# Optimization experiments

Measured on AMD Instinct MI355X. Metric: run time of the kernel, lower is better.

The kernel has to match this reference:

```python
import jax, jax.numpy as jnp
import numpy as np
from jax import lax


def conv1x1(x, w, b):
    # x: [B,C,H,W], w: [O,C], b: [O]
    return jnp.einsum('bchw,oc->bohw', x, w) + b[None, :, None, None]


def dwconv3(x, w, b):
    # depthwise 3x3, SAME padding. x: [B,C,H,W], w: [C,1,3,3], b: [C]
    C = x.shape[1]
    y = lax.conv_general_dilated(x, w, (1, 1), 'SAME',
                                 dimension_numbers=('NCHW', 'OIHW', 'NCHW'),
                                 feature_group_count=C)
    return y + b[None, :, None, None]


def proj(x, w1, b1, wd, bd):
    return dwconv3(conv1x1(x, w1, b1), wd, bd)


def setup_inputs() -> dict:
    key = jax.random.key(0)
    B, C, H, W = 8, 96, 256, 256
    ks = jax.random.split(key, 32)
    s = 0.05

    def rn(k, shape, scale=s):
        return jax.random.normal(k, shape, dtype=jnp.float32) * scale

    inp = {
        'I1': jax.random.normal(ks[0], (B, H * W, C), dtype=jnp.float32),
        'I2': jax.random.normal(ks[1], (B, H * W, C), dtype=jnp.float32),
        'h': H, 'w': W,
        'se1_w': rn(ks[2], (C, C)), 'se1_b': rn(ks[3], (C,)),
        'se1_dw': rn(ks[4], (C, 1, 3, 3)), 'se1_db': rn(ks[5], (C,)),
        'se2_w': rn(ks[6], (C, C)), 'se2_b': rn(ks[7], (C,)),
        'se2_dw': rn(ks[8], (C, 1, 3, 3)), 'se2_db': rn(ks[9], (C,)),
        'lp1_w': rn(ks[10], (C, C)), 'lp1_b': rn(ks[11], (C,)),
        'lp1_dw': rn(ks[12], (C, 1, 3, 3)), 'lp1_db': rn(ks[13], (C,)),
        'rp1_w': rn(ks[14], (C, C)), 'rp1_b': rn(ks[15], (C,)),
        'rp1_dw': rn(ks[16], (C, 1, 3, 3)), 'rp1_db': rn(ks[17], (C,)),
        'lp2_w': rn(ks[18], (C, C)), 'lp2_b': rn(ks[19], (C,)),
        'rp2_w': rn(ks[20], (C, C)), 'rp2_b': rn(ks[21], (C,)),
        'down_w': rn(ks[22], (C, 2 * C)), 'down_b': rn(ks[23], (C,)),
        'beta': rn(ks[24], (1, C, 1, 1), 0.1),
        'gamma': rn(ks[25], (1, C, 1, 1), 0.1),
    }
    return inp


def reference(I1, I2, h, w, se1_w, se1_b, se1_dw, se1_db, se2_w, se2_b,
              se2_dw, se2_db, lp1_w, lp1_b, lp1_dw, lp1_db, rp1_w, rp1_b,
              rp1_dw, rp1_db, lp2_w, lp2_b, rp2_w, rp2_b, down_w, down_b,
              beta, gamma):
    B, HW, C = I1.shape
    scale = C ** (-0.5)
    # PatchUnEmbed: [B, HW, C] -> [B, C, h, w]
    x_l = jnp.transpose(I1, (0, 2, 1)).reshape(B, C, h, w)
    x_r = jnp.transpose(I2, (0, 2, 1)).reshape(B, C, h, w)

    Q_l = jnp.transpose(proj(x_l, se1_w, se1_b, se1_dw, se1_db), (0, 2, 3, 1))  # [B,H,W,C]
    Q_r = jnp.transpose(proj(x_r, se2_w, se2_b, se2_dw, se2_db), (0, 2, 3, 1))  # [B,H,W,C]
    V_l = jnp.transpose(proj(x_l, lp1_w, lp1_b, lp1_dw, lp1_db), (0, 2, 3, 1))
    V_r = jnp.transpose(proj(x_r, rp1_w, rp1_b, rp1_dw, rp1_db), (0, 2, 3, 1))

    # row-wise cross attention along width: [B,H,W,W]
    attn = jax.nn.softmax(jnp.einsum('bhwc,bhvc->bhwv', Q_l, Q_r), axis=-1) * scale
    F_r2l = jnp.einsum('bhwv,bhvc->bhwc', attn, V_r)  # [B,H,W,C]
    F_l2r = jnp.einsum('bhwv,bhwc->bhvc', attn, V_l)  # attn^T @ V_l

    F_r2l = conv1x1(jnp.transpose(F_r2l, (0, 3, 1, 2)), lp2_w, lp2_b) * beta
    F_l2r = conv1x1(jnp.transpose(F_l2r, (0, 3, 1, 2)), rp2_w, rp2_b) * gamma

    fuse = conv1x1(jnp.concatenate([x_l + F_r2l, x_r + F_l2r], axis=1), down_w, down_b)
    # [B,C,H,W] -> [B, HW, C]
    return jnp.transpose(fuse.reshape(B, C, HW), (0, 2, 1))
```

## Files before the change

kernel.cpp:

```cpp
#include <hip/hip_runtime.h>
#include <hip/hip_bf16.h>
#include <stdint.h>

typedef __bf16 bf;
typedef __bf16 bfv8 __attribute__((ext_vector_type(8)));
typedef __bf16 bfv4 __attribute__((ext_vector_type(4)));
typedef float  f32x4 __attribute__((ext_vector_type(4)));

#define MFMA16(a,b,c) __builtin_amdgcn_mfma_f32_16x16x32_bf16((a),(b),(c),0,0,0)

#define CH  96
#define WID 256
#define HGT 256
#define NB  8
#define SCALE 0.1020620726159658f

__device__ __forceinline__ float b2f(bf x){ return (float)x; }
__device__ __forceinline__ bf   f2b(float x){ return (bf)x; }

__device__ __forceinline__ bfv8 ld_cvt8(const float* __restrict__ p){
  f32x4 a = *(const f32x4*)p;
  f32x4 b = *(const f32x4*)(p + 4);
  bfv8 r;
  r[0]=f2b(a[0]); r[1]=f2b(a[1]); r[2]=f2b(a[2]); r[3]=f2b(a[3]);
  r[4]=f2b(b[0]); r[5]=f2b(b[1]); r[6]=f2b(b[2]); r[7]=f2b(b[3]);
  return r;
}

__global__ __launch_bounds__(256) void k_c1x1(
    const float* __restrict__ X,
    const float* __restrict__ Wa, const float* __restrict__ Ba,
    const float* __restrict__ Wb, const float* __restrict__ Bb,
    bf* __restrict__ Ca, bf* __restrict__ Cb)
{
  const int tid=threadIdx.x, lane=tid&63, wv=tid>>6;
  const int l15=lane&15, lg=lane>>4;
  const int set = wv&1, th = wv>>1;
  const float* W1 = set ? Wb : Wa;
  const float* B1 = set ? Bb : Ba;
  bf* C = set ? Cb : Ca;
  const size_t p0 = (size_t)blockIdx.x * 256;

  bfv8 wf[6][3];
  float bias[6];
#pragma unroll
  for (int nt=0;nt<6;++nt){
    bias[nt] = B1[nt*16+l15];
#pragma unroll
    for (int ks=0;ks<3;++ks)
      wf[nt][ks] = ld_cvt8(W1 + (nt*16+l15)*CH + ks*32 + lg*8);
  }

#pragma unroll 1
  for (int i=0;i<8;++i){
    const int m0 = (th*8+i)*16;
    bfv8 af[3];
#pragma unroll
    for (int ks=0;ks<3;++ks)
      af[ks] = ld_cvt8(X + (p0+m0+l15)*CH + ks*32 + lg*8);
    f32x4 acc[6];
#pragma unroll
    for (int nt=0;nt<6;++nt) acc[nt]=(f32x4){bias[nt],bias[nt],bias[nt],bias[nt]};
#pragma unroll
    for (int ks=0;ks<3;++ks)
#pragma unroll
      for (int nt=0;nt<6;++nt)
        acc[nt] = MFMA16(af[ks], wf[nt][ks], acc[nt]);
#pragma unroll
    for (int nt=0;nt<6;++nt){
      int c = nt*16 + l15;
#pragma unroll
      for (int r=0;r<4;++r)
        C[(p0+m0+lg*4+r)*CH + c] = f2b(acc[nt][r]);
    }
  }
}

__global__ __launch_bounds__(256) void k_dw(
    const bf* __restrict__ C0, const bf* __restrict__ C1,
    const float* __restrict__ WD0, const float* __restrict__ BD0,
    const float* __restrict__ WD1, const float* __restrict__ BD1,
    bf* __restrict__ O0, bf* __restrict__ O1)
{
  const int tid = threadIdx.x;
  if (tid >= 240) return;
  const int g = tid % 12, slot = tid / 12;
  const int yrow = slot >> 2, xrun = slot & 3;
  const int b = blockIdx.z >> 1, s = blockIdx.z & 1;
  const bf* C = s ? C1 : C0;
  const float* WD = s ? WD1 : WD0;
  const float* BD = s ? BD1 : BD0;
  bf* O = s ? O1 : O0;
  const int x0 = blockIdx.x*64 + xrun*16;
  const int y  = blockIdx.y*5 + yrow;
  if (y >= HGT) return;
  const size_t ib = (size_t)b * (HGT*WID) * CH;

  float wv[9][8], bb[8];
#pragma unroll
  for (int j=0;j<8;++j){
    bb[j] = BD[g*8+j];
#pragma unroll
    for (int t=0;t<9;++t) wv[t][j] = WD[(g*8+j)*9 + t];
  }

  const bf* r0 = C + ib + ((size_t)(y-1)*WID)*CH + g*8;
  const bf* r1 = C + ib + ((size_t)(y  )*WID)*CH + g*8;
  const bf* r2 = C + ib + ((size_t)(y+1)*WID)*CH + g*8;
  const bool v0 = (y > 0), v2 = (y+1 < HGT);
  const bfv8 Z = {0,0,0,0,0,0,0,0};

  bfv8 w00,w01,w02, w10,w11,w12, w20,w21,w22;
  {
    bool vx = (x0 > 0);
    size_t o = (size_t)(x0-1)*CH;
    w00 = (v0&&vx) ? *(const bfv8*)(r0+o) : Z;
    w10 = vx       ? *(const bfv8*)(r1+o) : Z;
    w20 = (v2&&vx) ? *(const bfv8*)(r2+o) : Z;
  }
  {
    size_t o = (size_t)x0*CH;
    w01 = v0 ? *(const bfv8*)(r0+o) : Z;
    w11 =      *(const bfv8*)(r1+o);
    w21 = v2 ? *(const bfv8*)(r2+o) : Z;
  }
#pragma unroll
  for (int xi=0; xi<16; ++xi){
    const int xn = x0 + xi + 1;
    const bool vx = (xn < WID);
    const size_t o = (size_t)xn*CH;
    w02 = (v0&&vx) ? *(const bfv8*)(r0+o) : Z;
    w12 = vx       ? *(const bfv8*)(r1+o) : Z;
    w22 = (v2&&vx) ? *(const bfv8*)(r2+o) : Z;
    float acc[8];
#pragma unroll
    for (int j=0;j<8;++j) acc[j] = bb[j];
#pragma unroll
    for (int j=0;j<8;++j){
      acc[j] += wv[0][j]*b2f(w00[j]);
      acc[j] += wv[1][j]*b2f(w01[j]);
      acc[j] += wv[2][j]*b2f(w02[j]);
      acc[j] += wv[3][j]*b2f(w10[j]);
      acc[j] += wv[4][j]*b2f(w11[j]);
      acc[j] += wv[5][j]*b2f(w12[j]);
      acc[j] += wv[6][j]*b2f(w20[j]);
      acc[j] += wv[7][j]*b2f(w21[j]);
      acc[j] += wv[8][j]*b2f(w22[j]);
    }
    bfv8 st;
#pragma unroll
    for (int j=0;j<8;++j) st[j] = f2b(acc[j]);
    *(bfv8*)(O + ib + ((size_t)y*WID + x0 + xi)*CH + g*8) = st;
    w00=w01; w01=w02;
    w10=w11; w11=w12;
    w20=w21; w21=w22;
  }
}

__global__ __launch_bounds__(256) void k_attn(
    const bf* __restrict__ Ql, const bf* __restrict__ Qr,
    const bf* __restrict__ Vl, const bf* __restrict__ Vr,
    bf* __restrict__ Fout)
{
  extern __shared__ char sm[];
  bf* vt = (bf*)sm;
  bf* aq = (bf*)(sm + 96*264*2);
  float* rs = (float*)(sm + 96*264*2 + 4*16*104*2);
  const int tid=threadIdx.x, lane=tid&63, wid=tid>>6;
  const int l15=lane&15, lg=lane>>4;
  bf* aqw = aq + wid*(16*104);
  const int bh = blockIdx.x;
  const size_t qoff = (size_t)bh * (WID*CH);

#pragma unroll 1
  for (int phase=0; phase<2; ++phase) {
    const bf* msrc = phase ? Qr+qoff : Ql+qoff;
    const bf* nsrc = phase ? Ql+qoff : Qr+qoff;
    const bf* V    = (phase ? Vl : Vr) + qoff;
    const int outoff = phase ? CH : 0;
    if (phase) {
      __syncthreads();
      rs[tid] = SCALE / rs[tid];
    }
    {
      const bfv8* src = (const bfv8*)(V + (size_t)tid*CH);
#pragma unroll
      for (int i=0;i<12;++i){
        bfv8 v8 = src[i];
#pragma unroll
        for (int j=0;j<8;++j) vt[(i*8+j)*264 + tid] = v8[j];
      }
    }
    __syncthreads();

#pragma unroll 1
    for (int qp=0; qp<2; ++qp){
      bfv8 af2[2][3];
#pragma unroll
      for (int q01=0;q01<2;++q01){
        const int m0 = (qp*2+q01)*64 + wid*16;
#pragma unroll
        for (int ks=0;ks<3;++ks)
          af2[q01][ks] = *(const bfv8*)(msrc + (size_t)(m0+l15)*CH + ks*32 + lg*8);
      }
      f32x4 o[2][6];
#pragma unroll
      for (int q01=0;q01<2;++q01)
#pragma unroll
        for (int nt=0;nt<6;++nt) o[q01][nt]=(f32x4){0.f,0.f,0.f,0.f};
      float rsum[2][4]={{0.f,0.f,0.f,0.f},{0.f,0.f,0.f,0.f}};

#pragma unroll 1
      for (int c4=0;c4<4;++c4){
        bfv8 nb[4][3];
#pragma unroll
        for (int nt=0;nt<4;++nt)
#pragma unroll
          for (int ks=0;ks<3;++ks)
            nb[nt][ks] = *(const bfv8*)(nsrc + (size_t)(c4*64+nt*16+l15)*CH + ks*32+lg*8);
        float fwv[4];
        if (phase){
#pragma unroll
          for (int nt=0;nt<4;++nt) fwv[nt] = rs[c4*64+nt*16+l15];
        }
#pragma unroll
        for (int q01=0;q01<2;++q01){
          f32x4 acc[4];
#pragma unroll
          for (int nt=0;nt<4;++nt) acc[nt]=(f32x4){0.f,0.f,0.f,0.f};
#pragma unroll
          for (int ks=0;ks<3;++ks)
#pragma unroll
            for (int nt=0;nt<4;++nt)
              acc[nt]=MFMA16(af2[q01][ks], nb[nt][ks], acc[nt]);
          if (phase==0){
#pragma unroll
            for (int nt=0;nt<4;++nt)
#pragma unroll
              for (int r=0;r<4;++r){
                float e=__expf(acc[nt][r]); rsum[q01][r]+=e;
                aqw[(lg*4+r)*104 + nt*16+l15] = f2b(e);
              }
          } else {
#pragma unroll
            for (int nt=0;nt<4;++nt){
#pragma unroll
              for (int r=0;r<4;++r)
                aqw[(lg*4+r)*104 + nt*16+l15] = f2b(__expf(acc[nt][r])*fwv[nt]);
            }
          }
#pragma unroll
          for (int ks=0;ks<2;++ks){
            bfv8 aa = *(const bfv8*)(aqw + l15*104 + ks*32 + lg*8);
#pragma unroll
            for (int nt=0;nt<6;++nt)
              o[q01][nt]=MFMA16(aa,
                *(const bfv8*)(vt + (nt*16+l15)*264 + c4*64 + ks*32 + lg*8), o[q01][nt]);
          }
        }
      }
#pragma unroll
      for (int q01=0;q01<2;++q01){
        const int m0 = (qp*2+q01)*64 + wid*16;
        float sc[4];
        if (phase==0){
#pragma unroll
          for (int off=1; off<16; off<<=1)
#pragma unroll
            for (int r=0;r<4;++r) rsum[q01][r]+=__shfl_xor(rsum[q01][r],off,64);
          if (l15==0){
#pragma unroll
            for (int r=0;r<4;++r) rs[m0+lg*4+r]=rsum[q01][r];
          }
#pragma unroll
          for (int r=0;r<4;++r) sc[r]=SCALE/rsum[q01][r];
        } else {
#pragma unroll
          for (int r=0;r<4;++r) sc[r]=1.f;
        }
#pragma unroll
        for (int nt=0;nt<6;++nt)
#pragma unroll
          for (int r=0;r<4;++r)
            aqw[(lg*4+r)*104 + nt*16+l15] = f2b(o[q01][nt][r]*sc[r]);
        const size_t pbase=(size_t)bh*WID + m0;
#pragma unroll
        for (int i=0;i<3;++i){
          int u=lane+64*i; int gr=u/12, sg=u%12;
          *(bfv8*)(Fout + (pbase+gr)*192 + outoff + sg*8)
            = *(const bfv8*)(aqw + gr*104 + sg*8);
        }
      }
    }
  }
}

__global__ __launch_bounds__(256) void k_wprep(
    const float* __restrict__ L, const float* __restrict__ lb,
    const float* __restrict__ R, const float* __restrict__ rb,
    const float* __restrict__ D, const float* __restrict__ db,
    const float* __restrict__ beta, const float* __restrict__ gamma,
    bf* __restrict__ Wcat, float* __restrict__ bv)
{
  const int o = blockIdx.x;
  const int tid = threadIdx.x;
  for (int k = tid; k < 384; k += 256){
    float v;
    if (k < 192) v = D[o*192 + k];
    else if (k < 288){
      int c = k - 192; float s = 0.f;
      for (int m=0;m<96;++m) s += D[o*192+m]*beta[m]*L[m*96+c];
      v = s;
    } else {
      int c = k - 288; float s = 0.f;
      for (int m=0;m<96;++m) s += D[o*192+96+m]*gamma[m]*R[m*96+c];
      v = s;
    }
    Wcat[o*384+k] = f2b(v);
  }
  if (tid == 0){
    float s = db[o];
    for (int m=0;m<96;++m) s += D[o*192+m]*beta[m]*lb[m] + D[o*192+96+m]*gamma[m]*rb[m];
    bv[o] = s;
  }
}

__global__ __launch_bounds__(256) void k_fuse(
    const float* __restrict__ I1, const float* __restrict__ I2,
    const bf* F, const bf* __restrict__ Wcat, const float* __restrict__ bv,
    float* OUT)
{
  extern __shared__ bf fls[];
  const int tid=threadIdx.x, lane=tid&63, wv=tid>>6;
  const int l15=lane&15, lg=lane>>4;
  const int half = wv&1, pair = wv>>1;
  const size_t p0 = (size_t)blockIdx.x * 128;

  {
    const int row = tid>>1, seg = (tid&1)*96;
    const bf* fsrc = F + (p0+row)*192 + seg;
    bf* ldst = fls + row*200 + seg;
#pragma unroll
    for (int i=0;i<12;++i) *(bfv8*)(ldst + i*8) = *(const bfv8*)(fsrc + i*8);
  }

  bfv8 wf[12][3];
  float bias[3];
#pragma unroll
  for (int j=0;j<3;++j){
    int c = (half*3+j)*16 + l15;
    bias[j] = bv[c];
#pragma unroll
    for (int kb=0;kb<12;++kb)
      wf[kb][j] = *(const bfv8*)(Wcat + (size_t)c*384 + kb*32 + lg*8);
  }
  __syncthreads();

#pragma unroll
  for (int i=0;i<4;++i){
    const int mloc = (pair*4+i)*16;
    const size_t m0 = p0 + mloc;
    bfv8 a[12];
    const float* x1 = I1 + (m0+l15)*CH + lg*8;
    const float* x2 = I2 + (m0+l15)*CH + lg*8;
    const bf* fp = fls + (mloc+l15)*200 + lg*8;
#pragma unroll
    for (int ks=0;ks<3;++ks){
      a[ks]   = ld_cvt8(x1 + ks*32);
      a[3+ks] = ld_cvt8(x2 + ks*32);
      a[6+ks] = *(const bfv8*)(fp + ks*32);
      a[9+ks] = *(const bfv8*)(fp + 96 + ks*32);
    }
    f32x4 acc[3];
#pragma unroll
    for (int j=0;j<3;++j) acc[j]=(f32x4){bias[j],bias[j],bias[j],bias[j]};
#pragma unroll
    for (int kb=0;kb<12;++kb)
#pragma unroll
      for (int j=0;j<3;++j)
        acc[j] = MFMA16(a[kb], wf[kb][j], acc[j]);
#pragma unroll
    for (int j=0;j<3;++j){
      int c = (half*3+j)*16 + l15;
#pragma unroll
      for (int r=0;r<4;++r)
        OUT[(m0+lg*4+r)*CH + c] = acc[j][r];
    }
  }
}

extern "C" void kernel_launch(void* const* d_in, const int* in_sizes, int n_in,
                              void* d_out, int out_size, void* d_ws, size_t ws_size,
                              hipStream_t stream)
{
  (void)in_sizes; (void)n_in; (void)out_size; (void)ws_size;
  const float* I1 = (const float*)d_in[0];
  const float* I2 = (const float*)d_in[1];
  const float* se1_w = (const float*)d_in[4];
  const float* se1_b = (const float*)d_in[5];
  const float* se1_dw= (const float*)d_in[6];
  const float* se1_db= (const float*)d_in[7];
  const float* se2_w = (const float*)d_in[8];
  const float* se2_b = (const float*)d_in[9];
  const float* se2_dw= (const float*)d_in[10];
  const float* se2_db= (const float*)d_in[11];
  const float* lp1_w = (const float*)d_in[12];
  const float* lp1_b = (const float*)d_in[13];
  const float* lp1_dw= (const float*)d_in[14];
  const float* lp1_db= (const float*)d_in[15];
  const float* rp1_w = (const float*)d_in[16];
  const float* rp1_b = (const float*)d_in[17];
  const float* rp1_dw= (const float*)d_in[18];
  const float* rp1_db= (const float*)d_in[19];
  const float* lp2_w = (const float*)d_in[20];
  const float* lp2_b = (const float*)d_in[21];
  const float* rp2_w = (const float*)d_in[22];
  const float* rp2_b = (const float*)d_in[23];
  const float* down_w= (const float*)d_in[24];
  const float* down_b= (const float*)d_in[25];
  const float* beta  = (const float*)d_in[26];
  const float* gamma = (const float*)d_in[27];
  float* OUT = (float*)d_out;
  bf* Fbuf = (bf*)d_out;

  const size_t FIELD = (size_t)NB * HGT * WID * CH;
  bf* Ql = (bf*)d_ws;
  bf* Qr = Ql + FIELD;
  bf* Vl = Qr + FIELD;
  bf* Vr = Vl + FIELD;
  bf* Wcat = Vr + FIELD;
  float* bv = (float*)(Wcat + 96*384);
  bf* Cq = (bf*)d_out;
  bf* Cv = Cq + FIELD;

  dim3 blk(256,1,1);
  k_wprep<<<dim3(96,1,1), blk, 0, stream>>>(lp2_w, lp2_b, rp2_w, rp2_b,
        down_w, down_b, beta, gamma, Wcat, bv);
  k_c1x1<<<dim3(2048,1,1), blk, 0, stream>>>(I1, se1_w, se1_b, lp1_w, lp1_b, Cq, Cv);
  k_dw  <<<dim3(4,52,16),  blk, 0, stream>>>(Cq, Cv, se1_dw, se1_db, lp1_dw, lp1_db, Ql, Vl);
  k_c1x1<<<dim3(2048,1,1), blk, 0, stream>>>(I2, se2_w, se2_b, rp1_w, rp1_b, Cq, Cv);
  k_dw  <<<dim3(4,52,16),  blk, 0, stream>>>(Cq, Cv, se2_dw, se2_db, rp1_dw, rp1_db, Qr, Vr);

  k_attn<<<dim3(NB*HGT,1,1), blk, 96*264*2 + 4*16*104*2 + 256*4, stream>>>(
        Ql, Qr, Vl, Vr, Fbuf);
  k_fuse<<<dim3(4096,1,1), blk, 128*200*2, stream>>>(I1, I2, Fbuf, Wcat, bv, OUT);
}
```

Baseline: 1.076 ms.

## Swap MFMA operands for transposed accumulator layout and vectorized stores; prefetch inputs

Swaps the A/B operands of the MFMA calls in the 1x1 conv, attention and fuse kernels. Each lane's accumulator then holds four consecutive output channels (or keys) of one row, so results are written with packed bf16x4 or float4 stores instead of scalar strided stores. Bias and row-sum loads become vector loads, and the softmax row-sum reduction shrinks to two cross-lane shuffles. It also software-prefetches the next A tile in the 1x1 conv and the next column in the depthwise conv, at the cost of more registers per thread.

Result: faster. 1.031 ms (-4.2%).

```diff
diff --git a/kernel.cpp b/kernel.cpp
--- a/kernel.cpp
+++ b/kernel.cpp
@@ -26,6 +26,9 @@
   r[4]=f2b(b[0]); r[5]=f2b(b[1]); r[6]=f2b(b[2]); r[7]=f2b(b[3]);
   return r;
 }
+__device__ __forceinline__ bfv4 pack4(float a,float b,float c,float d){
+  bfv4 r; r[0]=f2b(a); r[1]=f2b(b); r[2]=f2b(c); r[3]=f2b(d); return r;
+}
 
 __global__ __launch_bounds__(256) void k_c1x1(
     const float* __restrict__ X,
@@ -42,37 +45,41 @@
   const size_t p0 = (size_t)blockIdx.x * 256;
 
   bfv8 wf[6][3];
-  float bias[6];
+  f32x4 bias4[6];
 #pragma unroll
   for (int nt=0;nt<6;++nt){
-    bias[nt] = B1[nt*16+l15];
+    bias4[nt] = *(const f32x4*)(B1 + nt*16 + lg*4);
 #pragma unroll
     for (int ks=0;ks<3;++ks)
       wf[nt][ks] = ld_cvt8(W1 + (nt*16+l15)*CH + ks*32 + lg*8);
   }
 
+  bfv8 af[3], afn[3];
+#pragma unroll
+  for (int ks=0;ks<3;++ks)
+    af[ks] = ld_cvt8(X + (p0 + th*8*16 + l15)*CH + ks*32 + lg*8);
 #pragma unroll 1
   for (int i=0;i<8;++i){
     const int m0 = (th*8+i)*16;
-    bfv8 af[3];
+    if (i<7){
+#pragma unroll
+      for (int ks=0;ks<3;++ks)
+        afn[ks] = ld_cvt8(X + (p0+m0+16+l15)*CH + ks*32 + lg*8);
+    }
+    f32x4 acc[6];
+#pragma unroll
+    for (int nt=0;nt<6;++nt) acc[nt]=bias4[nt];
 #pragma unroll
     for (int ks=0;ks<3;++ks)
-      af[ks] = ld_cvt8(X + (p0+m0+l15)*CH + ks*32 + lg*8);
-    f32x4 acc[6];
-#pragma unroll
-    for (int nt=0;nt<6;++nt) acc[nt]=(f32x4){bias[nt],bias[nt],bias[nt],bias[nt]};
-#pragma unroll
-    for (int ks=0;ks<3;++ks)
 #pragma unroll
       for (int nt=0;nt<6;++nt)
-        acc[nt] = MFMA16(af[ks], wf[nt][ks], acc[nt]);
-#pragma unroll
-    for (int nt=0;nt<6;++nt){
-      int c = nt*16 + l15;
-#pragma unroll
-      for (int r=0;r<4;++r)
-        C[(p0+m0+lg*4+r)*CH + c] = f2b(acc[nt][r]);
-    }
+        acc[nt] = MFMA16(wf[nt][ks], af[ks], acc[nt]);
+#pragma unroll
+    for (int nt=0;nt<6;++nt)
+      *(bfv4*)(C + (p0+m0+l15)*CH + nt*16 + lg*4)
+        = pack4(acc[nt][0],acc[nt][1],acc[nt][2],acc[nt][3]);
+#pragma unroll
+    for (int ks=0;ks<3;++ks) af[ks]=afn[ks];
   }
 }
 
@@ -110,7 +117,7 @@
   const bool v0 = (y > 0), v2 = (y+1 < HGT);
   const bfv8 Z = {0,0,0,0,0,0,0,0};
 
-  bfv8 w00,w01,w02, w10,w11,w12, w20,w21,w22;
+  bfv8 w00,w01,w02, w10,w11,w12, w20,w21,w22, n0,n1,n2;
   {
     bool vx = (x0 > 0);
     size_t o = (size_t)(x0-1)*CH;
@@ -124,14 +131,24 @@
     w11 =      *(const bfv8*)(r1+o);
     w21 = v2 ? *(const bfv8*)(r2+o) : Z;
   }
+  {
+    int xn = x0+1; bool vx = (xn < WID);
+    size_t o = (size_t)xn*CH;
+    n0 = (v0&&vx) ? *(const bfv8*)(r0+o) : Z;
+    n1 = vx       ? *(const bfv8*)(r1+o) : Z;
+    n2 = (v2&&vx) ? *(const bfv8*)(r2+o) : Z;
+  }
 #pragma unroll
   for (int xi=0; xi<16; ++xi){
-    const int xn = x0 + xi + 1;
-    const bool vx = (xn < WID);
-    const size_t o = (size_t)xn*CH;
-    w02 = (v0&&vx) ? *(const bfv8*)(r0+o) : Z;
-    w12 = vx       ? *(const bfv8*)(r1+o) : Z;
-    w22 = (v2&&vx) ? *(const bfv8*)(r2+o) : Z;
+    w02 = n0; w12 = n1; w22 = n2;
+    {
+      int xn2 = x0 + xi + 2;
+      bool vx2 = (xn2 < WID) && (xi < 15);
+      size_t o = (size_t)xn2*CH;
+      n0 = (v0&&vx2) ? *(const bfv8*)(r0+o) : Z;
+      n1 = vx2       ? *(const bfv8*)(r1+o) : Z;
+      n2 = (v2&&vx2) ? *(const bfv8*)(r2+o) : Z;
+    }
     float acc[8];
 #pragma unroll
     for (int j=0;j<8;++j) acc[j] = bb[j];
@@ -208,7 +225,7 @@
       for (int q01=0;q01<2;++q01)
 #pragma unroll
         for (int nt=0;nt<6;++nt) o[q01][nt]=(f32x4){0.f,0.f,0.f,0.f};
-      float rsum[2][4]={{0.f,0.f,0.f,0.f},{0.f,0.f,0.f,0.f}};
+      float rsum2[2]={0.f,0.f};
 
 #pragma unroll 1
       for (int c4=0;c4<4;++c4){
@@ -218,10 +235,11 @@
 #pragma unroll
           for (int ks=0;ks<3;++ks)
             nb[nt][ks] = *(const bfv8*)(nsrc + (size_t)(c4*64+nt*16+l15)*CH + ks*32+lg*8);
-        float fwv[4];
+        f32x4 fwv4[4];
         if (phase){
 #pragma unroll
-          for (int nt=0;nt<4;++nt) fwv[nt] = rs[c4*64+nt*16+l15];
+          for (int nt=0;nt<4;++nt)
+            fwv4[nt] = *(const f32x4*)(rs + c4*64 + nt*16 + lg*4);
         }
 #pragma unroll
         for (int q01=0;q01<2;++q01){
@@ -232,21 +250,23 @@
           for (int ks=0;ks<3;++ks)
 #pragma unroll
             for (int nt=0;nt<4;++nt)
-              acc[nt]=MFMA16(af2[q01][ks], nb[nt][ks], acc[nt]);
+              acc[nt]=MFMA16(nb[nt][ks], af2[q01][ks], acc[nt]);
           if (phase==0){
 #pragma unroll
-            for (int nt=0;nt<4;++nt)
-#pragma unroll
-              for (int r=0;r<4;++r){
-                float e=__expf(acc[nt][r]); rsum[q01][r]+=e;
-                aqw[(lg*4+r)*104 + nt*16+l15] = f2b(e);
-              }
+            for (int nt=0;nt<4;++nt){
+              float e0=__expf(acc[nt][0]), e1=__expf(acc[nt][1]);
+              float e2=__expf(acc[nt][2]), e3=__expf(acc[nt][3]);
+              rsum2[q01] += (e0+e1)+(e2+e3);
+              *(bfv4*)(aqw + l15*104 + nt*16 + lg*4) = pack4(e0,e1,e2,e3);
+            }
           } else {
 #pragma unroll
             for (int nt=0;nt<4;++nt){
-#pragma unroll
-              for (int r=0;r<4;++r)
-                aqw[(lg*4+r)*104 + nt*16+l15] = f2b(__expf(acc[nt][r])*fwv[nt]);
+              float e0=__expf(acc[nt][0])*fwv4[nt][0];
+              float e1=__expf(acc[nt][1])*fwv4[nt][1];
+              float e2=__expf(acc[nt][2])*fwv4[nt][2];
+              float e3=__expf(acc[nt][3])*fwv4[nt][3];
+              *(bfv4*)(aqw + l15*104 + nt*16 + lg*4) = pack4(e0,e1,e2,e3);
             }
           }
 #pragma unroll
@@ -254,35 +274,28 @@
             bfv8 aa = *(const bfv8*)(aqw + l15*104 + ks*32 + lg*8);
 #pragma unroll
             for (int nt=0;nt<6;++nt)
-              o[q01][nt]=MFMA16(aa,
-                *(const bfv8*)(vt + (nt*16+l15)*264 + c4*64 + ks*32 + lg*8), o[q01][nt]);
+              o[q01][nt]=MFMA16(
+                *(const bfv8*)(vt + (nt*16+l15)*264 + c4*64 + ks*32 + lg*8),
+                aa, o[q01][nt]);
           }
         }
       }
 #pragma unroll
       for (int q01=0;q01<2;++q01){
         const int m0 = (qp*2+q01)*64 + wid*16;
-        float sc[4];
+        float sc;
         if (phase==0){
-#pragma unroll
-          for (int off=1; off<16; off<<=1)
-#pragma unroll
-            for (int r=0;r<4;++r) rsum[q01][r]+=__shfl_xor(rsum[q01][r],off,64);
-          if (l15==0){
-#pragma unroll
-            for (int r=0;r<4;++r) rs[m0+lg*4+r]=rsum[q01][r];
-          }
-#pragma unroll
-          for (int r=0;r<4;++r) sc[r]=SCALE/rsum[q01][r];
-        } else {
-#pragma unroll
-          for (int r=0;r<4;++r) sc[r]=1.f;
-        }
+          float rsv = rsum2[q01];
+          rsv += __shfl_xor(rsv, 16, 64);
+          rsv += __shfl_xor(rsv, 32, 64);
+          if (lane < 16) rs[m0 + l15] = rsv;
+          sc = SCALE / rsv;
+        } else sc = 1.f;
 #pragma unroll
         for (int nt=0;nt<6;++nt)
-#pragma unroll
-          for (int r=0;r<4;++r)
-            aqw[(lg*4+r)*104 + nt*16+l15] = f2b(o[q01][nt][r]*sc[r]);
+          *(bfv4*)(aqw + l15*104 + nt*16 + lg*4)
+            = pack4(o[q01][nt][0]*sc, o[q01][nt][1]*sc,
+                    o[q01][nt][2]*sc, o[q01][nt][3]*sc);
         const size_t pbase=(size_t)bh*WID + m0;
 #pragma unroll
         for (int i=0;i<3;++i){
@@ -345,14 +358,14 @@
   }
 
   bfv8 wf[12][3];
-  float bias[3];
+  f32x4 bias4[3];
 #pragma unroll
   for (int j=0;j<3;++j){
-    int c = (half*3+j)*16 + l15;
-    bias[j] = bv[c];
+    int c = (half*3+j)*16;
+    bias4[j] = *(const f32x4*)(bv + c + lg*4);
 #pragma unroll
     for (int kb=0;kb<12;++kb)
-      wf[kb][j] = *(const bfv8*)(Wcat + (size_t)c*384 + kb*32 + lg*8);
+      wf[kb][j] = *(const bfv8*)(Wcat + (size_t)(c+l15)*384 + kb*32 + lg*8);
   }
   __syncthreads();
 
@@ -373,19 +386,15 @@
     }
     f32x4 acc[3];
 #pragma unroll
-    for (int j=0;j<3;++j) acc[j]=(f32x4){bias[j],bias[j],bias[j],bias[j]};
+    for (int j=0;j<3;++j) acc[j]=bias4[j];
 #pragma unroll
     for (int kb=0;kb<12;++kb)
 #pragma unroll
       for (int j=0;j<3;++j)
-        acc[j] = MFMA16(a[kb], wf[kb][j], acc[j]);
-#pragma unroll
-    for (int j=0;j<3;++j){
-      int c = (half*3+j)*16 + l15;
-#pragma unroll
-      for (int r=0;r<4;++r)
-        OUT[(m0+lg*4+r)*CH + c] = acc[j][r];
-    }
+        acc[j] = MFMA16(wf[kb][j], a[kb], acc[j]);
+#pragma unroll
+    for (int j=0;j<3;++j)
+      *(f32x4*)(OUT + (m0+l15)*CH + (half*3+j)*16 + lg*4) = acc[j];
   }
 }
 
@@ -440,7 +449,6 @@
   k_dw  <<<dim3(4,52,16),  blk, 0, stream>>>(Cq, Cv, se1_dw, se1_db, lp1_dw, lp1_db, Ql, Vl);
   k_c1x1<<<dim3(2048,1,1), blk, 0, stream>>>(I2, se2_w, se2_b, rp1_w, rp1_b, Cq, Cv);
   k_dw  <<<dim3(4,52,16),  blk, 0, stream>>>(Cq, Cv, se2_dw, se2_db, rp1_dw, rp1_db, Qr, Vr);
-
   k_attn<<<dim3(NB*HGT,1,1), blk, 96*264*2 + 4*16*104*2 + 256*4, stream>>>(
         Ql, Qr, Vl, Vr, Fbuf);
   k_fuse<<<dim3(4096,1,1), blk, 128*200*2, stream>>>(I1, I2, Fbuf, Wcat, bv, OUT);
```
